# Kernel optimization log

Measured on AMD Instinct MI355X. Metric: run time of the kernel, lower is better.

The kernel has to match this reference:

```python
import jax, jax.numpy as jnp
import numpy as np

C, H, V, N, T = 1024, 256, 10000, 16, 256


def setup_inputs() -> dict:
    key = jax.random.key(0)
    ks = jax.random.split(key, 16)
    s = 1.0 / np.sqrt(H)
    rn = lambda k, shape, sc: (jax.random.normal(k, shape, dtype=jnp.float32) * sc)
    d = {}
    d["text"] = jax.random.randint(ks[0], (N, T), 0, V)
    d["start_emb"] = rn(ks[1], (C, H), 1.0)
    d["sw1"] = rn(ks[2], (H, H), s); d["sb1"] = jnp.zeros((H,), jnp.float32)
    d["sw2"] = rn(ks[3], (H, H), s); d["sb2"] = jnp.zeros((H,), jnp.float32)
    d["sw3"] = rn(ks[4], (H, 1), s); d["sb3"] = jnp.zeros((1,), jnp.float32)
    d["state_emb"] = rn(ks[5], (C, H), 1.0)
    d["tw1"] = rn(ks[6], (H, H), s); d["tb1"] = jnp.zeros((H,), jnp.float32)
    d["tw2"] = rn(ks[7], (H, H), s); d["tb2"] = jnp.zeros((H,), jnp.float32)
    d["tw3"] = rn(ks[8], (H, C), s); d["tb3"] = jnp.zeros((C,), jnp.float32)
    d["pre_emb"] = rn(ks[9], (C, H), 1.0)
    d["ew1"] = rn(ks[10], (H, H), s); d["eb1"] = jnp.zeros((H,), jnp.float32)
    d["ew2"] = rn(ks[11], (H, H), s); d["eb2"] = jnp.zeros((H,), jnp.float32)
    d["ew3"] = rn(ks[12], (H, V), s); d["eb3"] = jnp.zeros((V,), jnp.float32)
    return d


def _res(x, w1, b1, w2, b2):
    # ResidualLayerOld: relu(lin2(relu(lin1(x)))) + x
    return jax.nn.relu(jax.nn.relu(x @ w1 + b1) @ w2 + b2) + x


def reference(text, start_emb, sw1, sb1, sw2, sb2, sw3, sb3,
              state_emb, tw1, tb1, tw2, tb2, tw3, tb3,
              pre_emb, ew1, eb1, ew2, eb2, ew3, eb3):
    # start: [C] log p(z_0)
    start = jax.nn.log_softmax((_res(start_emb, sw1, sb1, sw2, sb2) @ sw3 + sb3)[:, 0])
    # transition: log_softmax over next state, then permute -> [next, prev]
    trans = jax.nn.log_softmax(_res(state_emb, tw1, tb1, tw2, tb2) @ tw3 + tb3, axis=-1).T
    # emission: log_softmax over vocab, permute -> [V, C]
    emit = jax.nn.log_softmax(_res(pre_emb, ew1, eb1, ew2, eb2) @ ew3 + eb3, axis=-1).T

    obs = emit[text]                      # [N, T, C] log p(x_t | z_t=c)
    alpha0 = start[None, :] + obs[:, 0]   # [N, C]

    def step(alpha, e_t):
        # log-semiring matvec: alpha'[n,j] = logsumexp_i alpha[n,i] + trans[j,i]
        a = jax.scipy.special.logsumexp(alpha[:, None, :] + trans[None, :, :], axis=-1) + e_t
        return a, None

    alpha, _ = jax.lax.scan(step, alpha0, jnp.swapaxes(obs, 0, 1)[1:])
    # evidence: logsumexp over final states, summed over batch (full lengths)
    return jax.scipy.special.logsumexp(alpha, axis=-1).sum()
```

## Files before the change

kernel.cpp:

```cpp
#include <hip/hip_runtime.h>
#include <hip/hip_bf16.h>
#include <cstddef>

#define CC 1024
#define HH 256
#define VV 10000
#define NN 16
#define TT 256
#define NB 16
#define NVB 40

typedef __attribute__((ext_vector_type(8))) short s8b;
typedef __attribute__((ext_vector_type(4))) float f32x4;
typedef __attribute__((ext_vector_type(4))) unsigned int u32x4;

__device__ __forceinline__ unsigned short f2bf(float f) {
    unsigned int b = __builtin_bit_cast(unsigned int, f);
    b += 0x7FFFu + ((b >> 16) & 1u);
    return (unsigned short)(b >> 16);
}
__device__ __forceinline__ float bf2f(unsigned short u) {
    return __builtin_bit_cast(float, ((unsigned int)u) << 16);
}

struct ResArgs { const float *x, *w1, *b1, *w2, *b2; float* o; };
struct ResArgs3 { ResArgs a[3]; };

__global__ __launch_bounds__(256) void k_res(ResArgs3 A)
{
    ResArgs R = A.a[blockIdx.y];
    const int r0 = blockIdx.x * 16;
    const int th = threadIdx.x;
    __shared__ float xs[256][24];
    __shared__ float hs[256][24];
    #pragma unroll
    for (int k = 0; k < 16; k++) xs[th][k] = R.x[(size_t)(r0 + k) * HH + th];
    __syncthreads();
    float acc[16];
    float b1v = R.b1[th];
    #pragma unroll
    for (int r = 0; r < 16; r++) acc[r] = b1v;
    for (int h = 0; h < HH; h++) {
        float w = R.w1[(size_t)h * HH + th];
        #pragma unroll
        for (int r = 0; r < 16; r++) acc[r] = fmaf(xs[h][r], w, acc[r]);
    }
    #pragma unroll
    for (int r = 0; r < 16; r++) hs[th][r] = fmaxf(acc[r], 0.f);
    __syncthreads();
    float b2v = R.b2[th];
    #pragma unroll
    for (int r = 0; r < 16; r++) acc[r] = b2v;
    for (int h = 0; h < HH; h++) {
        float w = R.w2[(size_t)h * HH + th];
        #pragma unroll
        for (int r = 0; r < 16; r++) acc[r] = fmaf(hs[h][r], w, acc[r]);
    }
    #pragma unroll
    for (int r = 0; r < 16; r++) {
        size_t idx = (size_t)(r0 + r) * HH + th;
        R.o[idx] = fmaxf(acc[r], 0.f) + R.x[idx];
    }
}

__global__ __launch_bounds__(256) void k_slog(const float* __restrict__ res_s,
                                              const float* __restrict__ sw3,
                                              const float* __restrict__ sb3,
                                              float* __restrict__ slog)
{
    __shared__ float wv[256];
    const int th = threadIdx.x;
    const int c = blockIdx.x * 256 + th;
    wv[th] = sw3[th];
    __syncthreads();
    const float* row = res_s + (size_t)c * HH;
    float acc = 0.f;
    for (int h = 0; h < HH; h++) acc = fmaf(row[h], wv[h], acc);
    slog[c] = acc + sb3[0];
}

__global__ __launch_bounds__(256) void k_pt(const float* __restrict__ res_t,
                                            const float* __restrict__ tw3,
                                            const float* __restrict__ tb3,
                                            unsigned short* __restrict__ PB)
{
    const int r0 = blockIdx.x * 4;
    const int th = threadIdx.x;
    __shared__ float rs[4][256];
    __shared__ float sred[256];
    for (int k = 0; k < 4; k++) rs[k][th] = res_t[(size_t)(r0 + k) * HH + th];
    __syncthreads();
    float acc[4][4];
    #pragma unroll
    for (int r = 0; r < 4; r++)
        #pragma unroll
        for (int q = 0; q < 4; q++) acc[r][q] = tb3[th + q * 256];
    for (int h = 0; h < HH; h++) {
        float w0 = tw3[(size_t)h * CC + th];
        float w1 = tw3[(size_t)h * CC + th + 256];
        float w2 = tw3[(size_t)h * CC + th + 512];
        float w3 = tw3[(size_t)h * CC + th + 768];
        #pragma unroll
        for (int r = 0; r < 4; r++) {
            float xv = rs[r][h];
            acc[r][0] = fmaf(xv, w0, acc[r][0]);
            acc[r][1] = fmaf(xv, w1, acc[r][1]);
            acc[r][2] = fmaf(xv, w2, acc[r][2]);
            acc[r][3] = fmaf(xv, w3, acc[r][3]);
        }
    }
    for (int r = 0; r < 4; r++) {
        float m = fmaxf(fmaxf(acc[r][0], acc[r][1]), fmaxf(acc[r][2], acc[r][3]));
        sred[th] = m; __syncthreads();
        for (int off = 128; off > 0; off >>= 1) { if (th < off) sred[th] = fmaxf(sred[th], sred[th + off]); __syncthreads(); }
        float rm = sred[0]; __syncthreads();
        float ssum = __expf(acc[r][0] - rm) + __expf(acc[r][1] - rm) + __expf(acc[r][2] - rm) + __expf(acc[r][3] - rm);
        sred[th] = ssum; __syncthreads();
        for (int off = 128; off > 0; off >>= 1) { if (th < off) sred[th] += sred[th + off]; __syncthreads(); }
        float inv = 1.0f / sred[0]; __syncthreads();
        #pragma unroll
        for (int q = 0; q < 4; q++) {
            float p = __expf(acc[r][q] - rm) * inv;
            PB[(size_t)(th + q * 256) * CC + (r0 + r)] = f2bf(p);
        }
    }
}

__global__ __launch_bounds__(256) void k_emitg(const float* __restrict__ res_e,
                                               const float* __restrict__ ew3,
                                               const float* __restrict__ eb3,
                                               unsigned short* __restrict__ emitT,
                                               float* __restrict__ epart2)
{
    const int vb = blockIdx.x, c0 = blockIdx.y * 64;
    const int th = threadIdx.x;
    const int w = th >> 6, l = th & 63;
    const int lhi = l >> 4, llo = l & 15;
    const int wv = w & 1, wc = w >> 1;

    __shared__ __align__(16) unsigned short ewT[64 * 256];
    __shared__ __align__(16) unsigned short rsb[64 * 256];
    __shared__ float ebl[64];
    __shared__ float wlse[4][2][16][2];

    {
        char* base = (char*)rsb;
        #pragma unroll
        for (int i = 0; i < 8; i++) {
            int g = i * 2048 + th * 8;
            int row = g >> 8, h0 = g & 255;
            const float* src = res_e + (size_t)(c0 + row) * HH + h0;
            float4 f0 = *(const float4*)(src);
            float4 f1 = *(const float4*)(src + 4);
            s8b pk;
            pk[0] = (short)f2bf(f0.x); pk[1] = (short)f2bf(f0.y);
            pk[2] = (short)f2bf(f0.z); pk[3] = (short)f2bf(f0.w);
            pk[4] = (short)f2bf(f1.x); pk[5] = (short)f2bf(f1.y);
            pk[6] = (short)f2bf(f1.z); pk[7] = (short)f2bf(f1.w);
            *(s8b*)(base + row * 512 + ((h0 * 2) ^ ((row & 7) << 4))) = pk;
        }
    }

    float rM = -1e30f, rS = 0.f;

    for (int r = 0; r < 4; r++) {
        const int v0r = vb * 256 + r * 64;
        __syncthreads();
        {
            int tv = th & 63;
            char* base = (char*)ewT;
            int rowoff = tv * 512;
            int key = (tv & 7) << 4;
            int vglob = v0r + tv;
            bool valid = vglob < VV;
            #pragma unroll 8
            for (int i = 0; i < 64; i++) {
                int h = (th >> 6) + i * 4;
                float x = valid ? ew3[(size_t)h * VV + vglob] : 0.f;
                *(unsigned short*)(base + rowoff + ((h * 2) ^ key)) = f2bf(x);
            }
        }
        if (th < 64) ebl[th] = (v0r + th < VV) ? eb3[v0r + th] : 0.f;
        __syncthreads();

        f32x4 acc[2][2] = {{{0,0,0,0},{0,0,0,0}},{{0,0,0,0},{0,0,0,0}}};
        const char* ea = (const char*)ewT;
        const char* rb = (const char*)rsb;
        const int arow0 = wv * 32 + llo, arow1 = wv * 32 + 16 + llo;
        const int brow0 = wc * 32 + llo, brow1 = wc * 32 + 16 + llo;
        const int akey0 = (arow0 & 7) << 4;
        const int bkey0 = (brow0 & 7) << 4;
        #pragma unroll
        for (int kt = 0; kt < 8; kt++) {
            int off = kt * 64 + lhi * 16;
            s8b a0 = *(const s8b*)(ea + arow0 * 512 + (off ^ akey0));
            s8b a1 = *(const s8b*)(ea + arow1 * 512 + (off ^ akey0));
            s8b b0 = *(const s8b*)(rb + brow0 * 512 + (off ^ bkey0));
            s8b b1 = *(const s8b*)(rb + brow1 * 512 + (off ^ bkey0));
            acc[0][0] = __builtin_amdgcn_mfma_f32_16x16x32_bf16(a0, b0, acc[0][0], 0, 0, 0);
            acc[0][1] = __builtin_amdgcn_mfma_f32_16x16x32_bf16(a0, b1, acc[0][1], 0, 0, 0);
            acc[1][0] = __builtin_amdgcn_mfma_f32_16x16x32_bf16(a1, b0, acc[1][0], 0, 0, 0);
            acc[1][1] = __builtin_amdgcn_mfma_f32_16x16x32_bf16(a1, b1, acc[1][1], 0, 0, 0);
        }

        float um[2], us[2];
        #pragma unroll
        for (int u = 0; u < 2; u++) {
            float vals[8];
            #pragma unroll
            for (int s = 0; s < 2; s++) {
                #pragma unroll
                for (int q = 0; q < 4; q++) {
                    int vloc = wv * 32 + s * 16 + lhi * 4 + q;
                    int vglob = v0r + vloc;
                    float logit = acc[s][u][q] + ebl[vloc];
                    bool valid = vglob < VV;
                    if (valid)
                        emitT[(size_t)vglob * CC + (c0 + wc * 32 + u * 16 + llo)] = f2bf(logit);
                    vals[s * 4 + q] = valid ? logit : -1e30f;
                }
            }
            float m = vals[0];
            #pragma unroll
            for (int e = 1; e < 8; e++) m = fmaxf(m, vals[e]);
            float ss = 0.f;
            #pragma unroll
            for (int e = 0; e < 8; e++) ss += __expf(vals[e] - m);
            #pragma unroll
            for (int o = 16; o < 64; o <<= 1) {
                float m2 = __shfl_xor(m, o);
                float s2 = __shfl_xor(ss, o);
                float nm = fmaxf(m, m2);
                ss = ss * __expf(m - nm) + s2 * __expf(m2 - nm);
                m = nm;
            }
            um[u] = m; us[u] = ss;
        }
        if (l < 16) {
            #pragma unroll
            for (int u = 0; u < 2; u++) {
                wlse[w][u][l][0] = um[u];
                wlse[w][u][l][1] = us[u];
            }
        }
        __syncthreads();
        if (th < 64) {
            int wc2 = th >> 5, u2 = (th >> 4) & 1, ll2 = th & 15;
            float m1 = wlse[2 * wc2][u2][ll2][0], s1 = wlse[2 * wc2][u2][ll2][1];
            float m2 = wlse[2 * wc2 + 1][u2][ll2][0], s2 = wlse[2 * wc2 + 1][u2][ll2][1];
            float nm = fmaxf(m1, m2);
            float ns = s1 * __expf(m1 - nm) + s2 * __expf(m2 - nm);
            float fm = fmaxf(rM, nm);
            rS = rS * __expf(rM - fm) + ns * __expf(nm - fm);
            rM = fm;
        }
    }
    if (th < 64) {
        epart2[((size_t)vb * CC + c0 + th) * 2]     = rM;
        epart2[((size_t)vb * CC + c0 + th) * 2 + 1] = rS;
    }
}

__global__ __launch_bounds__(256) void k_lse(const float* __restrict__ epart2,
                                             float* __restrict__ lse)
{
    int c = blockIdx.x * 256 + threadIdx.x;
    float M = -1e30f, S = 0.f;
    for (int vb = 0; vb < NVB; vb++) {
        float m  = epart2[((size_t)vb * CC + c) * 2];
        float s2 = epart2[((size_t)vb * CC + c) * 2 + 1];
        float nm = fmaxf(M, m);
        S = S * __expf(M - nm) + s2 * __expf(m - nm);
        M = nm;
    }
    lse[c] = M + __logf(S);
}

__device__ __forceinline__ void load_stage(const unsigned short* vbuf_t, int th, char* vl)
{
    const unsigned short* sb = vbuf_t + th * 8;
    s8b ch[8];
    #pragma unroll
    for (int c = 0; c < 8; c++)
        asm volatile("global_load_dwordx4 %0, %1, off sc0 sc1"
                     : "=v"(ch[c]) : "v"(sb + c * 2048));
    asm volatile("s_waitcnt vmcnt(0)" ::: "memory");
    __builtin_amdgcn_sched_barrier(0);
    for (;;) {
        unsigned int miss = 0u;
        #pragma unroll
        for (int c = 0; c < 8; c++) {
            u32x4 d = __builtin_bit_cast(u32x4, ch[c]);
            if (d[0] == 0xFFFFFFFFu || d[1] == 0xFFFFFFFFu ||
                d[2] == 0xFFFFFFFFu || d[3] == 0xFFFFFFFFu) miss |= 1u << c;
        }
        if (!__any(miss != 0u)) break;
        #pragma unroll
        for (int c = 0; c < 8; c++)
            if (miss & (1u << c))
                asm volatile("global_load_dwordx4 %0, %1, off sc0 sc1"
                             : "=v"(ch[c]) : "v"(sb + c * 2048));
        asm volatile("s_waitcnt vmcnt(0)" ::: "memory");
        __builtin_amdgcn_sched_barrier(0);
    }
    #pragma unroll
    for (int c = 0; c < 8; c++) {
        int ow = c * 4096 + th * 16;
        *(s8b*)(vl + (ow ^ (((ow >> 11) & 7) << 4))) = ch[c];
    }
}

__global__ void __launch_bounds__(256, 1) k_fwd(
    const unsigned short* __restrict__ PB,
    const unsigned short* __restrict__ emitT,
    const float* __restrict__ lse,
    const float* __restrict__ slog,
    const int* __restrict__ text,
    unsigned short* vbuf,
    float* __restrict__ outp)
{
    const int blk = blockIdx.x;
    const int th = threadIdx.x;
    const int w = th >> 6, l = th & 63;
    const int lhi = l >> 4, llo = l & 15;
    const int jglob = blk * 64 + w * 16 + llo;

    __shared__ int toks[NN * TT];
    __shared__ __align__(16) unsigned short vlds[NN * CC];
    __shared__ __align__(16) unsigned short vtile[16][72];
    __shared__ float swk[4];
    __shared__ float fin[16];

    for (int i = th; i < NN * TT; i += 256) toks[i] = text[i];

    s8b bfr[32];
    {
        const unsigned short* pbj = PB + (size_t)jglob * CC + lhi * 8;
        #pragma unroll
        for (int kt = 0; kt < 32; kt++)
            bfr[kt] = *(const s8b*)(pbj + kt * 32);
    }
    s8b ones;
    #pragma unroll
    for (int e = 0; e < 8; e++) ones[e] = (short)0x3F80;

    const float lse_j = lse[jglob];

    float x0 = slog[th], x1 = slog[th + 256], x2 = slog[th + 512], x3 = slog[th + 768];
    float mw = fmaxf(fmaxf(x0, x1), fmaxf(x2, x3));
    #pragma unroll
    for (int o = 32; o; o >>= 1) mw = fmaxf(mw, __shfl_xor(mw, o));
    __syncthreads();
    if (l == 0) swk[w] = mw;
    __syncthreads();
    float gm = fmaxf(fmaxf(swk[0], swk[1]), fmaxf(swk[2], swk[3]));
    __syncthreads();
    float e4 = __expf(x0 - gm) + __expf(x1 - gm) + __expf(x2 - gm) + __expf(x3 - gm);
    #pragma unroll
    for (int o = 32; o; o >>= 1) e4 += __shfl_xor(e4, o);
    if (l == 0) swk[w] = e4;
    __syncthreads();
    float slse = gm + __logf(swk[0] + swk[1] + swk[2] + swk[3]);
    __syncthreads();

    if (th < 64) {
        int jj = blk * 64 + th;
        float p0 = __expf(slog[jj] - slse);
        float lsej = lse[jj];
        #pragma unroll
        for (int n = 0; n < 16; n++)
            vtile[n][th] = f2bf(p0 * __expf(bf2f(emitT[(size_t)toks[n * TT] * CC + jj]) - lsej));
    }
    __syncthreads();
    if (th < 128) {
        int n = th >> 3, seg = th & 7;
        s8b val = *(const s8b*)&vtile[n][seg * 8];
        unsigned short* dst = vbuf + (size_t)n * CC + blk * 64 + seg * 8;
        asm volatile("global_store_dwordx4 %0, %1, off sc0 sc1" :: "v"(dst), "v"(val) : "memory");
    }

    float logaccq[4] = {0.f, 0.f, 0.f, 0.f};
    char* vl = (char*)vlds;
    const int rkey = (llo & 7) << 4;
    const int rbase = llo * 2048 + lhi * 16;

    for (int t = 1; t < TT; t++) {
        float epf[4];
        #pragma unroll
        for (int q = 0; q < 4; q++)
            epf[q] = __expf(bf2f(emitT[(size_t)toks[(lhi * 4 + q) * TT + t] * CC + jglob]) - lse_j);

        load_stage(vbuf + (size_t)(t - 1) * (NN * CC), th, vl);
        __syncthreads();

        f32x4 ac0 = {0,0,0,0}, ac1 = {0,0,0,0}, ac2 = {0,0,0,0}, ac3 = {0,0,0,0};
        f32x4 ao0 = {0,0,0,0}, ao1 = {0,0,0,0};
        #pragma unroll
        for (int kt = 0; kt < 32; kt += 4) {
            s8b a0 = *(const s8b*)(vl + ((rbase + (kt + 0) * 64) ^ rkey));
            s8b a1 = *(const s8b*)(vl + ((rbase + (kt + 1) * 64) ^ rkey));
            s8b a2 = *(const s8b*)(vl + ((rbase + (kt + 2) * 64) ^ rkey));
            s8b a3 = *(const s8b*)(vl + ((rbase + (kt + 3) * 64) ^ rkey));
            ac0 = __builtin_amdgcn_mfma_f32_16x16x32_bf16(a0, bfr[kt + 0], ac0, 0, 0, 0);
            ao0 = __builtin_amdgcn_mfma_f32_16x16x32_bf16(a0, ones,        ao0, 0, 0, 0);
            ac1 = __builtin_amdgcn_mfma_f32_16x16x32_bf16(a1, bfr[kt + 1], ac1, 0, 0, 0);
            ao1 = __builtin_amdgcn_mfma_f32_16x16x32_bf16(a1, ones,        ao1, 0, 0, 0);
            ac2 = __builtin_amdgcn_mfma_f32_16x16x32_bf16(a2, bfr[kt + 2], ac2, 0, 0, 0);
            ao0 = __builtin_amdgcn_mfma_f32_16x16x32_bf16(a2, ones,        ao0, 0, 0, 0);
            ac3 = __builtin_amdgcn_mfma_f32_16x16x32_bf16(a3, bfr[kt + 3], ac3, 0, 0, 0);
            ao1 = __builtin_amdgcn_mfma_f32_16x16x32_bf16(a3, ones,        ao1, 0, 0, 0);
        }
        f32x4 acc = (ac0 + ac1) + (ac2 + ac3);
        f32x4 aco = ao0 + ao1;

        #pragma unroll
        for (int q = 0; q < 4; q++) {
            float S = aco[q];
            logaccq[q] += __logf(S);
            float vq = acc[q] * (1.0f / S) * epf[q];
            vtile[lhi * 4 + q][w * 16 + llo] = f2bf(vq);
        }
        __syncthreads();

        if (th < 128) {
            int n = th >> 3, seg = th & 7;
            s8b val = *(const s8b*)&vtile[n][seg * 8];
            unsigned short* dst = vbuf + (size_t)t * (NN * CC) + (size_t)n * CC + blk * 64 + seg * 8;
            asm volatile("global_store_dwordx4 %0, %1, off sc0 sc1" :: "v"(dst), "v"(val) : "memory");
        }
    }

    if (blk == 0) {
        load_stage(vbuf + (size_t)255 * (NN * CC), th, vl);
        __syncthreads();
        f32x4 ao0 = {0,0,0,0}, ao1 = {0,0,0,0};
        #pragma unroll
        for (int kt = 0; kt < 32; kt += 2) {
            s8b a0 = *(const s8b*)(vl + ((rbase + (kt + 0) * 64) ^ rkey));
            s8b a1 = *(const s8b*)(vl + ((rbase + (kt + 1) * 64) ^ rkey));
            ao0 = __builtin_amdgcn_mfma_f32_16x16x32_bf16(a0, ones, ao0, 0, 0, 0);
            ao1 = __builtin_amdgcn_mfma_f32_16x16x32_bf16(a1, ones, ao1, 0, 0, 0);
        }
        f32x4 acoF = ao0 + ao1;
        if (w == 0 && llo == 0) {
            #pragma unroll
            for (int q = 0; q < 4; q++)
                fin[lhi * 4 + q] = logaccq[q] + __logf(acoF[q]);
        }
        __syncthreads();
        if (th == 0) {
            float tot = 0.f;
            for (int n = 0; n < 16; n++) tot += fin[n];
            outp[0] = tot;
        }
    }
}

extern "C" void kernel_launch(void* const* d_in, const int* in_sizes, int n_in,
                              void* d_out, int out_size, void* d_ws, size_t ws_size,
                              hipStream_t stream) {
    const int*   text      = (const int*)  d_in[0];
    const float* start_emb = (const float*)d_in[1];
    const float* sw1 = (const float*)d_in[2];
    const float* sb1 = (const float*)d_in[3];
    const float* sw2 = (const float*)d_in[4];
    const float* sb2 = (const float*)d_in[5];
    const float* sw3 = (const float*)d_in[6];
    const float* sb3 = (const float*)d_in[7];
    const float* state_emb = (const float*)d_in[8];
    const float* tw1 = (const float*)d_in[9];
    const float* tb1 = (const float*)d_in[10];
    const float* tw2 = (const float*)d_in[11];
    const float* tb2 = (const float*)d_in[12];
    const float* tw3 = (const float*)d_in[13];
    const float* tb3 = (const float*)d_in[14];
    const float* pre_emb = (const float*)d_in[15];
    const float* ew1 = (const float*)d_in[16];
    const float* eb1 = (const float*)d_in[17];
    const float* ew2 = (const float*)d_in[18];
    const float* eb2 = (const float*)d_in[19];
    const float* ew3 = (const float*)d_in[20];
    const float* eb3 = (const float*)d_in[21];

    char* wsp = (char*)d_ws;
    unsigned short* PB    = (unsigned short*)(wsp);
    unsigned short* emitT = (unsigned short*)(wsp + ((size_t)2 << 20));
    float* res_s = (float*)(wsp + ((size_t)2 << 20));
    float* res_t = (float*)(wsp + ((size_t)3 << 20));
    float* res_e = (float*)(wsp + 22577152u);
    float* slog  = (float*)(wsp + 23625728u);
    float* lse   = (float*)(wsp + 23629824u);
    float* epart2= (float*)(wsp + 23633920u);
    unsigned short* vbuf = (unsigned short*)(wsp + ((size_t)23 << 20));
    float* outp  = (float*)d_out;

    if (ws_size < ((size_t)31 << 20)) return;

    hipMemsetAsync(vbuf, 0xFF, (size_t)TT * NN * CC * sizeof(unsigned short), stream);

    ResArgs3 ra;
    ra.a[0] = { start_emb, sw1, sb1, sw2, sb2, res_s };
    ra.a[1] = { state_emb, tw1, tb1, tw2, tb2, res_t };
    ra.a[2] = { pre_emb,   ew1, eb1, ew2, eb2, res_e };

    hipLaunchKernelGGL(k_res,   dim3(64, 3),   dim3(256), 0, stream, ra);
    hipLaunchKernelGGL(k_slog,  dim3(4),       dim3(256), 0, stream, res_s, sw3, sb3, slog);
    hipLaunchKernelGGL(k_pt,    dim3(256),     dim3(256), 0, stream, res_t, tw3, tb3, PB);
    hipLaunchKernelGGL(k_emitg, dim3(NVB, 16), dim3(256), 0, stream, res_e, ew3, eb3, emitT, epart2);
    hipLaunchKernelGGL(k_lse,   dim3(4),       dim3(256), 0, stream, epart2, lse);
    hipLaunchKernelGGL(k_fwd,   dim3(NB),      dim3(256), 0, stream,
                       PB, emitT, lse, slog, text, vbuf, outp);
}
```

Measured before the change: 957.7 us.

## Fuse prep kernels and vbuf init into one launch, fold lse into forward

Replaces the residual MLP, start-logit, transition-softmax and vbuf memset launches with a single heterogeneous kernel whose block ranges handle each job. The start and transition residual MLPs are now computed in place inside the blocks that consume them, and the start projection becomes a wave-shuffle reduction. The separate lse kernel is removed and its per-column log-sum-exp merge now runs at the start of the forward kernel. This cuts launch count and serialization between small kernels. In exchange, the 256 transition blocks each recompute only 4 rows of the residual MLP, which uses less reuse, and the forward kernel takes on extra startup work.

```diff
diff --git a/kernel.cpp b/kernel.cpp
--- a/kernel.cpp
+++ b/kernel.cpp
@@ -23,106 +23,171 @@
     return __builtin_bit_cast(float, ((unsigned int)u) << 16);
 }
 
-struct ResArgs { const float *x, *w1, *b1, *w2, *b2; float* o; };
-struct ResArgs3 { ResArgs a[3]; };
-
-__global__ __launch_bounds__(256) void k_res(ResArgs3 A)
+__global__ __launch_bounds__(256) void k_prep(
+    const float* __restrict__ start_emb,
+    const float* __restrict__ sw1, const float* __restrict__ sb1,
+    const float* __restrict__ sw2, const float* __restrict__ sb2,
+    const float* __restrict__ sw3, const float* __restrict__ sb3,
+    const float* __restrict__ state_emb,
+    const float* __restrict__ tw1, const float* __restrict__ tb1,
+    const float* __restrict__ tw2, const float* __restrict__ tb2,
+    const float* __restrict__ tw3, const float* __restrict__ tb3,
+    const float* __restrict__ pre_emb,
+    const float* __restrict__ ew1, const float* __restrict__ eb1,
+    const float* __restrict__ ew2, const float* __restrict__ eb2,
+    float* __restrict__ res_e, float* __restrict__ slog,
+    unsigned short* __restrict__ PB, unsigned short* __restrict__ vbuf)
 {
-    ResArgs R = A.a[blockIdx.y];
-    const int r0 = blockIdx.x * 16;
-    const int th = threadIdx.x;
     __shared__ float xs[256][24];
     __shared__ float hs[256][24];
-    #pragma unroll
-    for (int k = 0; k < 16; k++) xs[th][k] = R.x[(size_t)(r0 + k) * HH + th];
-    __syncthreads();
-    float acc[16];
-    float b1v = R.b1[th];
-    #pragma unroll
-    for (int r = 0; r < 16; r++) acc[r] = b1v;
-    for (int h = 0; h < HH; h++) {
-        float w = R.w1[(size_t)h * HH + th];
-        #pragma unroll
-        for (int r = 0; r < 16; r++) acc[r] = fmaf(xs[h][r], w, acc[r]);
-    }
-    #pragma unroll
-    for (int r = 0; r < 16; r++) hs[th][r] = fmaxf(acc[r], 0.f);
-    __syncthreads();
-    float b2v = R.b2[th];
-    #pragma unroll
-    for (int r = 0; r < 16; r++) acc[r] = b2v;
-    for (int h = 0; h < HH; h++) {
-        float w = R.w2[(size_t)h * HH + th];
-        #pragma unroll
-        for (int r = 0; r < 16; r++) acc[r] = fmaf(hs[h][r], w, acc[r]);
-    }
-    #pragma unroll
-    for (int r = 0; r < 16; r++) {
-        size_t idx = (size_t)(r0 + r) * HH + th;
-        R.o[idx] = fmaxf(acc[r], 0.f) + R.x[idx];
-    }
-}
-
-__global__ __launch_bounds__(256) void k_slog(const float* __restrict__ res_s,
-                                              const float* __restrict__ sw3,
-                                              const float* __restrict__ sb3,
-                                              float* __restrict__ slog)
-{
-    __shared__ float wv[256];
     const int th = threadIdx.x;
-    const int c = blockIdx.x * 256 + th;
-    wv[th] = sw3[th];
-    __syncthreads();
-    const float* row = res_s + (size_t)c * HH;
-    float acc = 0.f;
-    for (int h = 0; h < HH; h++) acc = fmaf(row[h], wv[h], acc);
-    slog[c] = acc + sb3[0];
-}
-
-__global__ __launch_bounds__(256) void k_pt(const float* __restrict__ res_t,
-                                            const float* __restrict__ tw3,
-                                            const float* __restrict__ tb3,
-                                            unsigned short* __restrict__ PB)
-{
-    const int r0 = blockIdx.x * 4;
-    const int th = threadIdx.x;
-    __shared__ float rs[4][256];
-    __shared__ float sred[256];
-    for (int k = 0; k < 4; k++) rs[k][th] = res_t[(size_t)(r0 + k) * HH + th];
-    __syncthreads();
-    float acc[4][4];
-    #pragma unroll
-    for (int r = 0; r < 4; r++)
-        #pragma unroll
-        for (int q = 0; q < 4; q++) acc[r][q] = tb3[th + q * 256];
-    for (int h = 0; h < HH; h++) {
-        float w0 = tw3[(size_t)h * CC + th];
-        float w1 = tw3[(size_t)h * CC + th + 256];
-        float w2 = tw3[(size_t)h * CC + th + 512];
-        float w3 = tw3[(size_t)h * CC + th + 768];
-        #pragma unroll
+    const int b = blockIdx.x;
+
+    if (b < 64) {
+        const int r0 = b * 16;
+        #pragma unroll
+        for (int k = 0; k < 16; k++) xs[th][k] = pre_emb[(size_t)(r0 + k) * HH + th];
+        __syncthreads();
+        float acc[16];
+        float b1v = eb1[th];
+        #pragma unroll
+        for (int r = 0; r < 16; r++) acc[r] = b1v;
+        for (int h = 0; h < HH; h++) {
+            float w = ew1[(size_t)h * HH + th];
+            #pragma unroll
+            for (int r = 0; r < 16; r++) acc[r] = fmaf(xs[h][r], w, acc[r]);
+        }
+        #pragma unroll
+        for (int r = 0; r < 16; r++) hs[th][r] = fmaxf(acc[r], 0.f);
+        __syncthreads();
+        float b2v = eb2[th];
+        #pragma unroll
+        for (int r = 0; r < 16; r++) acc[r] = b2v;
+        for (int h = 0; h < HH; h++) {
+            float w = ew2[(size_t)h * HH + th];
+            #pragma unroll
+            for (int r = 0; r < 16; r++) acc[r] = fmaf(hs[h][r], w, acc[r]);
+        }
+        #pragma unroll
+        for (int r = 0; r < 16; r++) {
+            size_t idx = (size_t)(r0 + r) * HH + th;
+            res_e[idx] = fmaxf(acc[r], 0.f) + pre_emb[idx];
+        }
+    } else if (b < 128) {
+        const int r0 = (b - 64) * 16;
+        #pragma unroll
+        for (int k = 0; k < 16; k++) xs[th][k] = start_emb[(size_t)(r0 + k) * HH + th];
+        __syncthreads();
+        float acc[16];
+        float b1v = sb1[th];
+        #pragma unroll
+        for (int r = 0; r < 16; r++) acc[r] = b1v;
+        for (int h = 0; h < HH; h++) {
+            float w = sw1[(size_t)h * HH + th];
+            #pragma unroll
+            for (int r = 0; r < 16; r++) acc[r] = fmaf(xs[h][r], w, acc[r]);
+        }
+        #pragma unroll
+        for (int r = 0; r < 16; r++) hs[th][r] = fmaxf(acc[r], 0.f);
+        __syncthreads();
+        float b2v = sb2[th];
+        #pragma unroll
+        for (int r = 0; r < 16; r++) acc[r] = b2v;
+        for (int h = 0; h < HH; h++) {
+            float w = sw2[(size_t)h * HH + th];
+            #pragma unroll
+            for (int r = 0; r < 16; r++) acc[r] = fmaf(hs[h][r], w, acc[r]);
+        }
+        float accf[16];
+        #pragma unroll
+        for (int r = 0; r < 16; r++)
+            accf[r] = fmaxf(acc[r], 0.f) + start_emb[(size_t)(r0 + r) * HH + th];
+        __syncthreads();
+        float* ws = (float*)&hs[0][0];
+        float wv = sw3[th];
+        const int wq = th >> 6, ln = th & 63;
+        #pragma unroll
+        for (int r = 0; r < 16; r++) {
+            float p = accf[r] * wv;
+            #pragma unroll
+            for (int o = 32; o; o >>= 1) p += __shfl_xor(p, o);
+            if (ln == 0) ws[wq * 16 + r] = p;
+        }
+        __syncthreads();
+        if (th < 16) slog[r0 + th] = ws[th] + ws[16 + th] + ws[32 + th] + ws[48 + th] + sb3[0];
+    } else if (b < 384) {
+        const int r0c = (b - 128) * 4;
+        float (*rs)[256] = (float (*)[256])&xs[0][0];
+        float (*h2)[256] = (float (*)[256])(&xs[0][0] + 1024);
+        float* sred = (float*)&hs[0][0];
+        for (int k = 0; k < 4; k++) rs[k][th] = state_emb[(size_t)(r0c + k) * HH + th];
+        __syncthreads();
+        float a1[4];
+        {
+            float b1v = tb1[th];
+            #pragma unroll
+            for (int r = 0; r < 4; r++) a1[r] = b1v;
+            for (int h = 0; h < HH; h++) {
+                float w = tw1[(size_t)h * HH + th];
+                #pragma unroll
+                for (int r = 0; r < 4; r++) a1[r] = fmaf(rs[r][h], w, a1[r]);
+            }
+        }
+        #pragma unroll
+        for (int r = 0; r < 4; r++) h2[r][th] = fmaxf(a1[r], 0.f);
+        __syncthreads();
+        float a2[4];
+        {
+            float b2v = tb2[th];
+            #pragma unroll
+            for (int r = 0; r < 4; r++) a2[r] = b2v;
+            for (int h = 0; h < HH; h++) {
+                float w = tw2[(size_t)h * HH + th];
+                #pragma unroll
+                for (int r = 0; r < 4; r++) a2[r] = fmaf(h2[r][h], w, a2[r]);
+            }
+        }
+        #pragma unroll
+        for (int r = 0; r < 4; r++) rs[r][th] = fmaxf(a2[r], 0.f) + rs[r][th];
+        __syncthreads();
+        float acc[4][4];
+        #pragma unroll
+        for (int r = 0; r < 4; r++)
+            #pragma unroll
+            for (int q = 0; q < 4; q++) acc[r][q] = tb3[th + q * 256];
+        for (int h = 0; h < HH; h++) {
+            float w0 = tw3[(size_t)h * CC + th];
+            float w1 = tw3[(size_t)h * CC + th + 256];
+            float w2 = tw3[(size_t)h * CC + th + 512];
+            float w3 = tw3[(size_t)h * CC + th + 768];
+            #pragma unroll
+            for (int r = 0; r < 4; r++) {
+                float xv = rs[r][h];
+                acc[r][0] = fmaf(xv, w0, acc[r][0]);
+                acc[r][1] = fmaf(xv, w1, acc[r][1]);
+                acc[r][2] = fmaf(xv, w2, acc[r][2]);
+                acc[r][3] = fmaf(xv, w3, acc[r][3]);
+            }
+        }
         for (int r = 0; r < 4; r++) {
-            float xv = rs[r][h];
-            acc[r][0] = fmaf(xv, w0, acc[r][0]);
-            acc[r][1] = fmaf(xv, w1, acc[r][1]);
-            acc[r][2] = fmaf(xv, w2, acc[r][2]);
-            acc[r][3] = fmaf(xv, w3, acc[r][3]);
-        }
-    }
-    for (int r = 0; r < 4; r++) {
-        float m = fmaxf(fmaxf(acc[r][0], acc[r][1]), fmaxf(acc[r][2], acc[r][3]));
-        sred[th] = m; __syncthreads();
-        for (int off = 128; off > 0; off >>= 1) { if (th < off) sred[th] = fmaxf(sred[th], sred[th + off]); __syncthreads(); }
-        float rm = sred[0]; __syncthreads();
-        float ssum = __expf(acc[r][0] - rm) + __expf(acc[r][1] - rm) + __expf(acc[r][2] - rm) + __expf(acc[r][3] - rm);
-        sred[th] = ssum; __syncthreads();
-        for (int off = 128; off > 0; off >>= 1) { if (th < off) sred[th] += sred[th + off]; __syncthreads(); }
-        float inv = 1.0f / sred[0]; __syncthreads();
-        #pragma unroll
-        for (int q = 0; q < 4; q++) {
-            float p = __expf(acc[r][q] - rm) * inv;
-            PB[(size_t)(th + q * 256) * CC + (r0 + r)] = f2bf(p);
-        }
+            float m = fmaxf(fmaxf(acc[r][0], acc[r][1]), fmaxf(acc[r][2], acc[r][3]));
+            sred[th] = m; __syncthreads();
+            for (int off = 128; off > 0; off >>= 1) { if (th < off) sred[th] = fmaxf(sred[th], sred[th + off]); __syncthreads(); }
+            float rm = sred[0]; __syncthreads();
+            float ssum = __expf(acc[r][0] - rm) + __expf(acc[r][1] - rm) + __expf(acc[r][2] - rm) + __expf(acc[r][3] - rm);
+            sred[th] = ssum; __syncthreads();
+            for (int off = 128; off > 0; off >>= 1) { if (th < off) sred[th] += sred[th + off]; __syncthreads(); }
+            float inv = 1.0f / sred[0]; __syncthreads();
+            #pragma unroll
+            for (int q = 0; q < 4; q++) {
+                float p = __expf(acc[r][q] - rm) * inv;
+                PB[(size_t)(th + q * 256) * CC + (r0c + r)] = f2bf(p);
+            }
+        }
+    } else {
+        const int blk = b - 384;
+        unsigned long long* dst = (unsigned long long*)vbuf + (size_t)blk * 16384;
+        for (int i = th; i < 16384; i += 256) dst[i] = 0xFFFFFFFFFFFFFFFFull;
     }
 }
 
@@ -261,21 +326,6 @@
     }
 }
 
-__global__ __launch_bounds__(256) void k_lse(const float* __restrict__ epart2,
-                                             float* __restrict__ lse)
-{
-    int c = blockIdx.x * 256 + threadIdx.x;
-    float M = -1e30f, S = 0.f;
-    for (int vb = 0; vb < NVB; vb++) {
-        float m  = epart2[((size_t)vb * CC + c) * 2];
-        float s2 = epart2[((size_t)vb * CC + c) * 2 + 1];
-        float nm = fmaxf(M, m);
-        S = S * __expf(M - nm) + s2 * __expf(m - nm);
-        M = nm;
-    }
-    lse[c] = M + __logf(S);
-}
-
 __device__ __forceinline__ void load_stage(const unsigned short* vbuf_t, int th, char* vl)
 {
     const unsigned short* sb = vbuf_t + th * 8;
@@ -313,7 +363,7 @@
 __global__ void __launch_bounds__(256, 1) k_fwd(
     const unsigned short* __restrict__ PB,
     const unsigned short* __restrict__ emitT,
-    const float* __restrict__ lse,
+    const float* __restrict__ epart2,
     const float* __restrict__ slog,
     const int* __restrict__ text,
     unsigned short* vbuf,
@@ -330,6 +380,7 @@
     __shared__ __align__(16) unsigned short vtile[16][72];
     __shared__ float swk[4];
     __shared__ float fin[16];
+    __shared__ float lsej[64];
 
     for (int i = th; i < NN * TT; i += 256) toks[i] = text[i];
 
@@ -344,7 +395,35 @@
     #pragma unroll
     for (int e = 0; e < 8; e++) ones[e] = (short)0x3F80;
 
-    const float lse_j = lse[jglob];
+    {
+        float* mm  = (float*)vlds;
+        float* ssm = mm + 256;
+        int cl = blk * 64 + (th & 63);
+        int v0 = (th >> 6) * 10;
+        float M = -1e30f, S = 0.f;
+        for (int vb = v0; vb < v0 + 10; vb++) {
+            float m  = epart2[((size_t)vb * CC + cl) * 2];
+            float s2 = epart2[((size_t)vb * CC + cl) * 2 + 1];
+            float nm = fmaxf(M, m);
+            S = S * __expf(M - nm) + s2 * __expf(m - nm);
+            M = nm;
+        }
+        mm[th] = M; ssm[th] = S;
+        __syncthreads();
+        if (th < 64) {
+            float Mf = -1e30f, Sf = 0.f;
+            #pragma unroll
+            for (int q = 0; q < 4; q++) {
+                float m = mm[q * 64 + th], s2 = ssm[q * 64 + th];
+                float nm = fmaxf(Mf, m);
+                Sf = Sf * __expf(Mf - nm) + s2 * __expf(m - nm);
+                Mf = nm;
+            }
+            lsej[th] = Mf + __logf(Sf);
+        }
+        __syncthreads();
+    }
+    const float lse_j = lsej[w * 16 + llo];
 
     float x0 = slog[th], x1 = slog[th + 256], x2 = slog[th + 512], x3 = slog[th + 768];
     float mw = fmaxf(fmaxf(x0, x1), fmaxf(x2, x3));
@@ -366,10 +445,10 @@
     if (th < 64) {
         int jj = blk * 64 + th;
         float p0 = __expf(slog[jj] - slse);
-        float lsej = lse[jj];
+        float lsej_c = lsej[th];
         #pragma unroll
         for (int n = 0; n < 16; n++)
-            vtile[n][th] = f2bf(p0 * __expf(bf2f(emitT[(size_t)toks[n * TT] * CC + jj]) - lsej));
+            vtile[n][th] = f2bf(p0 * __expf(bf2f(emitT[(size_t)toks[n * TT] * CC + jj]) - lsej_c));
     }
     __syncthreads();
     if (th < 128) {
@@ -485,29 +564,20 @@
     char* wsp = (char*)d_ws;
     unsigned short* PB    = (unsigned short*)(wsp);
     unsigned short* emitT = (unsigned short*)(wsp + ((size_t)2 << 20));
-    float* res_s = (float*)(wsp + ((size_t)2 << 20));
-    float* res_t = (float*)(wsp + ((size_t)3 << 20));
     float* res_e = (float*)(wsp + 22577152u);
     float* slog  = (float*)(wsp + 23625728u);
-    float* lse   = (float*)(wsp + 23629824u);
     float* epart2= (float*)(wsp + 23633920u);
     unsigned short* vbuf = (unsigned short*)(wsp + ((size_t)23 << 20));
     float* outp  = (float*)d_out;
 
     if (ws_size < ((size_t)31 << 20)) return;
 
-    hipMemsetAsync(vbuf, 0xFF, (size_t)TT * NN * CC * sizeof(unsigned short), stream);
-
-    ResArgs3 ra;
-    ra.a[0] = { start_emb, sw1, sb1, sw2, sb2, res_s };
-    ra.a[1] = { state_emb, tw1, tb1, tw2, tb2, res_t };
-    ra.a[2] = { pre_emb,   ew1, eb1, ew2, eb2, res_e };
-
-    hipLaunchKernelGGL(k_res,   dim3(64, 3),   dim3(256), 0, stream, ra);
-    hipLaunchKernelGGL(k_slog,  dim3(4),       dim3(256), 0, stream, res_s, sw3, sb3, slog);
-    hipLaunchKernelGGL(k_pt,    dim3(256),     dim3(256), 0, stream, res_t, tw3, tb3, PB);
+    hipLaunchKernelGGL(k_prep,  dim3(448),     dim3(256), 0, stream,
+                       start_emb, sw1, sb1, sw2, sb2, sw3, sb3,
+                       state_emb, tw1, tb1, tw2, tb2, tw3, tb3,
+                       pre_emb,   ew1, eb1, ew2, eb2,
+                       res_e, slog, PB, vbuf);
     hipLaunchKernelGGL(k_emitg, dim3(NVB, 16), dim3(256), 0, stream, res_e, ew3, eb3, emitT, epart2);
-    hipLaunchKernelGGL(k_lse,   dim3(4),       dim3(256), 0, stream, epart2, lse);
     hipLaunchKernelGGL(k_fwd,   dim3(NB),      dim3(256), 0, stream,
-                       PB, emitT, lse, slog, text, vbuf, outp);
-}
+                       PB, emitT, epart2, slog, text, vbuf, outp);
+}
```

New measurement: 914.7 us, median of 3. -4.5%, faster.
